# Optimization experiments

Hardware: AMD Instinct MI355X
Metric: run time of the kernel (lower is better)

Reference implementation:

```python
import jax, jax.numpy as jnp
import numpy as np

TOKENS = 8192
IN_F = 4096
OUT_F = 11008


def setup_inputs() -> dict:
    key = jax.random.key(0)
    k1, k2, k3, k4, k5 = jax.random.split(key, 5)
    x = jax.random.normal(k1, (TOKENS, IN_F), dtype=jnp.float32)
    # packed int4 weights: one int32 byte-value in [0,256) per pair of int4s
    weight_packed = jax.random.randint(k2, (IN_F, OUT_F // 2), 0, 256, dtype=jnp.int32)
    weight_scale = jax.random.uniform(k3, (OUT_F,), dtype=jnp.float32) * 0.02 + 1e-3
    weight_offset = jax.random.normal(k4, (OUT_F,), dtype=jnp.float32)  # stored as -offset, as in module
    bias = jax.random.normal(k5, (OUT_F,), dtype=jnp.float32)
    return {"x": x, "weight_packed": weight_packed, "weight_scale": weight_scale,
            "weight_offset": weight_offset, "bias": bias}


def _unpack_int4(weight_packed):
    # inverse of int42int8: low nibble = even column, high nibble = odd column,
    # both signed int4 in [-8, 7]. Sign-extend via (v ^ 8) - 8.
    low = ((weight_packed & 15) ^ 8) - 8
    high = (((weight_packed >> 4) & 15) ^ 8) - 8
    k = weight_packed.shape[0]
    q = jnp.stack([low, high], axis=-1).reshape(k, -1)  # [in, out]
    return q


def reference(x, weight_packed, weight_scale, weight_offset, bias):
    q = _unpack_int4(weight_packed).astype(jnp.float32)          # [in, out]
    w = (q + weight_offset[None, :]) * weight_scale[None, :]      # dequant: stored offset is -zero_point
    return x @ w + bias[None, :]                                  # [tokens, out]
```

## Files before the change

kernel.cpp:

```cpp
#include <hip/hip_runtime.h>
#include <stdint.h>

#define TOKENS 8192
#define IN_F   4096
#define OUT_F  11008
#define PACKED (OUT_F / 2)

typedef __bf16   bf16x8 __attribute__((ext_vector_type(8)));
typedef float    f32x4  __attribute__((ext_vector_type(4)));
typedef uint16_t u16x8  __attribute__((ext_vector_type(8)));

__device__ __forceinline__ uint16_t f32_to_bf16(float f) {
    union { float f; uint32_t u; } c; c.f = f;
    uint32_t r = c.u + 0x7FFFu + ((c.u >> 16) & 1u);
    return (uint16_t)(r >> 16);
}

__global__ __launch_bounds__(256) void xcvt_kernel(const float* __restrict__ x,
                                                   uint16_t* __restrict__ xb) {
    size_t base = ((size_t)blockIdx.x * 256 + threadIdx.x) * 8;
    float4 v0 = *(const float4*)(x + base);
    float4 v1 = *(const float4*)(x + base + 4);
    u16x8 o;
    o[0] = f32_to_bf16(v0.x); o[1] = f32_to_bf16(v0.y);
    o[2] = f32_to_bf16(v0.z); o[3] = f32_to_bf16(v0.w);
    o[4] = f32_to_bf16(v1.x); o[5] = f32_to_bf16(v1.y);
    o[6] = f32_to_bf16(v1.z); o[7] = f32_to_bf16(v1.w);
    *(u16x8*)(xb + base) = o;
}

#define WDQ_STRIDE 72
__global__ __launch_bounds__(256) void wdeq_kernel(const int* __restrict__ wp,
                                                   const float* __restrict__ woff,
                                                   uint16_t* __restrict__ wt) {
    __shared__ uint16_t tile[64 * WDQ_STRIDE];
    const int t  = threadIdx.x;
    const int p0 = blockIdx.y * 32;
    const int k0 = blockIdx.x * 64;
    const int pl = t & 31;
    const int kb = t >> 5;
    const int p  = p0 + pl;
    const float off_e = woff[2 * p];
    const float off_o = woff[2 * p + 1];
    #pragma unroll
    for (int j = 0; j < 8; ++j) {
        int kl = j * 8 + kb;
        int v  = wp[(size_t)(k0 + kl) * PACKED + p];
        int lo = ((v & 15) ^ 8) - 8;
        int hi = (((v >> 4) & 15) ^ 8) - 8;
        tile[(2 * pl)     * WDQ_STRIDE + kl] = f32_to_bf16((float)lo + off_e);
        tile[(2 * pl + 1) * WDQ_STRIDE + kl] = f32_to_bf16((float)hi + off_o);
    }
    __syncthreads();
    const int nl = t >> 2;
    const int kc = (t & 3) * 16;
    u16x8 w0 = *(const u16x8*)&tile[nl * WDQ_STRIDE + kc];
    u16x8 w1 = *(const u16x8*)&tile[nl * WDQ_STRIDE + kc + 8];
    uint16_t* dst = wt + (size_t)(2 * p0 + nl) * IN_F + k0 + kc;
    *(u16x8*)dst       = w0;
    *(u16x8*)(dst + 8) = w1;
}

#define CP16(ldsp, gp)                                                                        \
    __builtin_amdgcn_global_load_lds((const __attribute__((address_space(1))) void*)(gp),     \
                                     (__attribute__((address_space(3))) void*)(ldsp), 16, 0, 0)

__global__ __launch_bounds__(256) void gemm_kernel(const uint16_t* __restrict__ xb,
                                                   const uint16_t* __restrict__ wt,
                                                   const float* __restrict__ scale,
                                                   const float* __restrict__ bias,
                                                   float* __restrict__ out) {
    __shared__ uint16_t smem[8192];

    const int tid  = threadIdx.x;
    const int wid  = tid >> 6;
    const int lane = tid & 63;
    const int quad = lane >> 4;
    const int l15  = lane & 15;

    const int bm = blockIdx.x & 63;
    const int bn = blockIdx.x >> 6;
    const int m0 = bm << 7;
    const int n0 = bn << 7;
    const int wm = (wid >> 1) << 6;
    const int wn = (wid & 1) << 6;

    const int rowi = tid >> 2;
    const int kbyt = ((tid & 3) ^ (rowi & 3)) << 4;

    const char* ga0 = (const char*)(xb + (size_t)(m0 + rowi)      * IN_F) + kbyt;
    const char* ga1 = (const char*)(xb + (size_t)(m0 + rowi + 64) * IN_F) + kbyt;
    const char* gb0 = (const char*)(wt + (size_t)(n0 + rowi)      * IN_F) + kbyt;
    const char* gb1 = (const char*)(wt + (size_t)(n0 + rowi + 64) * IN_F) + kbyt;

    char* lds = (char*)smem;
    char* la0 = lds + wid * 1024;
    char* la1 = lds + 4096  + wid * 1024;
    char* lb0 = lds + 8192  + wid * 1024;
    char* lb1 = lds + 12288 + wid * 1024;

    const int arow = wm + l15;
    const int brow = wn + l15;
    const uint16_t* afrag = smem +        arow * 32 + ((quad ^ (arow & 3)) << 3);
    const uint16_t* bfrag = smem + 4096 + brow * 32 + ((quad ^ (brow & 3)) << 3);

    f32x4 acc[4][4] = {};

    for (int k0 = 0; k0 < IN_F; k0 += 32) {
        __syncthreads();
        CP16(la0, ga0); CP16(la1, ga1);
        CP16(lb0, gb0); CP16(lb1, gb1);
        ga0 += 64; ga1 += 64; gb0 += 64; gb1 += 64;
        __syncthreads();

        bf16x8 a[4], b[4];
        #pragma unroll
        for (int i = 0; i < 4; ++i) a[i] = *(const bf16x8*)(afrag + i * 512);
        #pragma unroll
        for (int i = 0; i < 4; ++i) b[i] = *(const bf16x8*)(bfrag + i * 512);
        #pragma unroll
        for (int mt = 0; mt < 4; ++mt)
            #pragma unroll
            for (int nt = 0; nt < 4; ++nt)
                acc[mt][nt] = __builtin_amdgcn_mfma_f32_16x16x32_bf16(a[mt], b[nt],
                                                                      acc[mt][nt], 0, 0, 0);
    }

    #pragma unroll
    for (int nt = 0; nt < 4; ++nt) {
        int n    = n0 + wn + nt * 16 + l15;
        float s  = scale[n];
        float bb = bias[n];
        #pragma unroll
        for (int mt = 0; mt < 4; ++mt) {
            int m = m0 + wm + mt * 16 + quad * 4;
            float* o = out + (size_t)m * OUT_F + n;
            #pragma unroll
            for (int r = 0; r < 4; ++r)
                o[(size_t)r * OUT_F] = acc[mt][nt][r] * s + bb;
        }
    }
}

extern "C" void kernel_launch(void* const* d_in, const int* in_sizes, int n_in,
                              void* d_out, int out_size, void* d_ws, size_t ws_size,
                              hipStream_t stream) {
    const float* x     = (const float*)d_in[0];
    const int*   wp    = (const int*)d_in[1];
    const float* scale = (const float*)d_in[2];
    const float* woff  = (const float*)d_in[3];
    const float* bias  = (const float*)d_in[4];
    float* out = (float*)d_out;

    uint16_t* xb = (uint16_t*)d_ws;
    uint16_t* wt = xb + (size_t)TOKENS * IN_F;

    xcvt_kernel<<<(TOKENS * (size_t)IN_F) / (256 * 8), 256, 0, stream>>>(x, xb);
    wdeq_kernel<<<dim3(IN_F / 64, PACKED / 32), 256, 0, stream>>>(wp, woff, wt);
    gemm_kernel<<<(TOKENS / 128) * (OUT_F / 128), 256, 0, stream>>>(xb, wt, scale, bias, out);
}
```

Before: 1.377 ms.

## Rewrite GEMM as 256x256 tile, 8-wave, double-buffered LDS pipeline with interleaved MFMA

```diff
diff --git a/kernel.cpp b/kernel.cpp
--- a/kernel.cpp
+++ b/kernel.cpp
@@ -5,6 +5,7 @@
 #define IN_F   4096
 #define OUT_F  11008
 #define PACKED (OUT_F / 2)
+#define NKT    (IN_F / 64)
 
 typedef __bf16   bf16x8 __attribute__((ext_vector_type(8)));
 typedef float    f32x4  __attribute__((ext_vector_type(4)));
@@ -61,83 +62,127 @@
     *(u16x8*)(dst + 8) = w1;
 }
 
+
 #define CP16(ldsp, gp)                                                                        \
     __builtin_amdgcn_global_load_lds((const __attribute__((address_space(1))) void*)(gp),     \
                                      (__attribute__((address_space(3))) void*)(ldsp), 16, 0, 0)
 
-__global__ __launch_bounds__(256) void gemm_kernel(const uint16_t* __restrict__ xb,
-                                                   const uint16_t* __restrict__ wt,
-                                                   const float* __restrict__ scale,
-                                                   const float* __restrict__ bias,
-                                                   float* __restrict__ out) {
-    __shared__ uint16_t smem[8192];
+#define STAGE2(ldsoff, gptr) {                                      \
+    CP16((char*)smem + (ldsoff),        (gptr));                    \
+    CP16((char*)smem + (ldsoff) + 8192, (gptr) + 262144); }
+
+#define FENCE() asm volatile("" ::: "memory")
+#define BAR()  { FENCE(); __builtin_amdgcn_s_barrier(); FENCE(); }
+
+#define LDA(MH) {                                                       \
+    _Pragma("unroll") for (int im = 0; im < 4; ++im) {                  \
+      a[im][0] = *(const bf16x8*)(Ard + ((MH)*4+im)*2048 + swz0);       \
+      a[im][1] = *(const bf16x8*)(Ard + ((MH)*4+im)*2048 + swz1); } }
+
+#define LDB(dst, NH) {                                                  \
+    _Pragma("unroll") for (int i2 = 0; i2 < 2; ++i2) {                  \
+      dst[i2][0] = *(const bf16x8*)(Brd + ((NH)*2+i2)*2048 + swz0);     \
+      dst[i2][1] = *(const bf16x8*)(Brd + ((NH)*2+i2)*2048 + swz1); } }
+
+#define MMA(MH, NH, B) {                                                \
+    __builtin_amdgcn_s_setprio(1);                                      \
+    _Pragma("unroll") for (int ik = 0; ik < 2; ++ik)                    \
+      _Pragma("unroll") for (int im = 0; im < 4; ++im)                  \
+        _Pragma("unroll") for (int i2 = 0; i2 < 2; ++i2)                \
+          acc[(MH)*4+im][(NH)*2+i2] = __builtin_amdgcn_mfma_f32_16x16x32_bf16( \
+              a[im][ik], B[i2][ik], acc[(MH)*4+im][(NH)*2+i2], 0, 0, 0); \
+    __builtin_amdgcn_s_setprio(0); }
+
+__global__ __launch_bounds__(512, 2) void gemm_kernel(const uint16_t* __restrict__ xb,
+                                                      const uint16_t* __restrict__ wt,
+                                                      const float* __restrict__ scale,
+                                                      const float* __restrict__ bias,
+                                                      float* __restrict__ out) {
+    __shared__ char smem[131072];
 
     const int tid  = threadIdx.x;
-    const int wid  = tid >> 6;
+    const int w    = tid >> 6;
     const int lane = tid & 63;
     const int quad = lane >> 4;
     const int l15  = lane & 15;
-
-    const int bm = blockIdx.x & 63;
-    const int bn = blockIdx.x >> 6;
-    const int m0 = bm << 7;
-    const int n0 = bn << 7;
-    const int wm = (wid >> 1) << 6;
-    const int wn = (wid & 1) << 6;
-
-    const int rowi = tid >> 2;
-    const int kbyt = ((tid & 3) ^ (rowi & 3)) << 4;
-
-    const char* ga0 = (const char*)(xb + (size_t)(m0 + rowi)      * IN_F) + kbyt;
-    const char* ga1 = (const char*)(xb + (size_t)(m0 + rowi + 64) * IN_F) + kbyt;
-    const char* gb0 = (const char*)(wt + (size_t)(n0 + rowi)      * IN_F) + kbyt;
-    const char* gb1 = (const char*)(wt + (size_t)(n0 + rowi + 64) * IN_F) + kbyt;
-
-    char* lds = (char*)smem;
-    char* la0 = lds + wid * 1024;
-    char* la1 = lds + 4096  + wid * 1024;
-    char* lb0 = lds + 8192  + wid * 1024;
-    char* lb1 = lds + 12288 + wid * 1024;
-
-    const int arow = wm + l15;
-    const int brow = wn + l15;
-    const uint16_t* afrag = smem +        arow * 32 + ((quad ^ (arow & 3)) << 3);
-    const uint16_t* bfrag = smem + 4096 + brow * 32 + ((quad ^ (brow & 3)) << 3);
-
-    f32x4 acc[4][4] = {};
-
-    for (int k0 = 0; k0 < IN_F; k0 += 32) {
-        __syncthreads();
-        CP16(la0, ga0); CP16(la1, ga1);
-        CP16(lb0, gb0); CP16(lb1, gb1);
-        ga0 += 64; ga1 += 64; gb0 += 64; gb1 += 64;
-        __syncthreads();
-
-        bf16x8 a[4], b[4];
+    const int wm   = w >> 2;
+    const int wn   = w & 3;
+
+    const int bm = blockIdx.x & 31;
+    const int bn = blockIdx.x >> 5;
+    const int m0 = bm << 8;
+    const int n0 = bn << 8;
+
+    const int srow = tid >> 3;
+    const int schk = (tid & 7) ^ (srow & 7);
+    const uint16_t* gA = xb + (size_t)(m0 + srow) * IN_F + schk * 8;
+    const uint16_t* gB = wt + (size_t)(n0 + srow) * IN_F + schk * 8;
+    const int wb = w * 1024;
+
+    const int swz0 = (( quad     ) ^ (l15 & 7)) * 16 + l15 * 128;
+    const int swz1 = ((quad + 4) ^ (l15 & 7)) * 16 + l15 * 128;
+
+    const char* lds = (const char*)smem;
+
+    STAGE2(65536 +                 wb, gB);
+    STAGE2(65536 + 16384 +         wb, gB + 524288);
+    STAGE2(                        wb, gA);
+    STAGE2(16384 +                 wb, gA + 524288);
+    STAGE2(65536 + 32768 +         wb, gB + 64);
+    STAGE2(65536 + 32768 + 16384 + wb, gB + 64 + 524288);
+    asm volatile("s_waitcnt vmcnt(4)" ::: "memory");
+    BAR();
+
+    f32x4  acc[8][4] = {};
+    bf16x8 a[4][2], b0[2][2], b1[2][2];
+
+    #pragma unroll 2
+    for (int kt = 0; kt < NKT; ++kt) {
+        const int p = kt & 1;
+        const char* Ard = lds + p * 32768 + wm * 16384;
+        const char* Brd = lds + 65536 + p * 32768 + (wn >> 1) * 16384 + (wn & 1) * 8192;
+        const int AstB = (p ^ 1) * 32768 + wb;
+        const int BstB = 65536 + p * 32768 + wb;
+        const bool stA = kt < NKT - 1;
+        const bool stB = kt < NKT - 2;
+
+        LDA(0); LDB(b0, 0);
+        if (stA) STAGE2(AstB, gA + 64);
+        BAR();
+        MMA(0, 0, b0);
+        BAR();
+        LDB(b1, 1);
+        if (stA) STAGE2(AstB + 16384, gA + 64 + 524288);
+        BAR();
+        MMA(0, 1, b1);
+        BAR();
+        LDA(1);
+        if (stB) STAGE2(BstB, gB + 128);
+        BAR();
+        MMA(1, 1, b1);
+        BAR();
+        if (stB) STAGE2(BstB + 16384, gB + 128 + 524288);
+        if (kt < NKT - 2)       { asm volatile("s_waitcnt vmcnt(4)" ::: "memory"); }
+        else if (kt == NKT - 2) { asm volatile("s_waitcnt vmcnt(0)" ::: "memory"); }
+        BAR();
+        MMA(1, 0, b0);
+        BAR();
+
+        gA += 64; gB += 64;
+    }
+
+    #pragma unroll
+    for (int nf = 0; nf < 4; ++nf) {
+        const int n    = n0 + wn * 64 + nf * 16 + l15;
+        const float s  = scale[n];
+        const float bb = bias[n];
         #pragma unroll
-        for (int i = 0; i < 4; ++i) a[i] = *(const bf16x8*)(afrag + i * 512);
-        #pragma unroll
-        for (int i = 0; i < 4; ++i) b[i] = *(const bf16x8*)(bfrag + i * 512);
-        #pragma unroll
-        for (int mt = 0; mt < 4; ++mt)
-            #pragma unroll
-            for (int nt = 0; nt < 4; ++nt)
-                acc[mt][nt] = __builtin_amdgcn_mfma_f32_16x16x32_bf16(a[mt], b[nt],
-                                                                      acc[mt][nt], 0, 0, 0);
-    }
-
-    #pragma unroll
-    for (int nt = 0; nt < 4; ++nt) {
-        int n    = n0 + wn + nt * 16 + l15;
-        float s  = scale[n];
-        float bb = bias[n];
-        #pragma unroll
-        for (int mt = 0; mt < 4; ++mt) {
-            int m = m0 + wm + mt * 16 + quad * 4;
+        for (int mf = 0; mf < 8; ++mf) {
+            const int m = m0 + wm * 128 + mf * 16 + quad * 4;
             float* o = out + (size_t)m * OUT_F + n;
             #pragma unroll
             for (int r = 0; r < 4; ++r)
-                o[(size_t)r * OUT_F] = acc[mt][nt][r] * s + bb;
+                o[(size_t)r * OUT_F] = acc[mf][nf][r] * s + bb;
         }
     }
 }
@@ -157,5 +202,5 @@
 
     xcvt_kernel<<<(TOKENS * (size_t)IN_F) / (256 * 8), 256, 0, stream>>>(x, xb);
     wdeq_kernel<<<dim3(IN_F / 64, PACKED / 32), 256, 0, stream>>>(wp, woff, wt);
-    gemm_kernel<<<(TOKENS / 128) * (OUT_F / 128), 256, 0, stream>>>(xb, wt, scale, bias, out);
-}
+    gemm_kernel<<<(TOKENS / 256) * (OUT_F / 256), 512, 0, stream>>>(xb, wt, scale, bias, out);
+}
```

Measured after the change: 1.137 ms. 17.4% less time.
